# Kernel tuning notes

Hardware: AMD Instinct MI355X
Metric: run time of the kernel (lower is better)

The kernel has to match this reference:

```python
import jax, jax.numpy as jnp
import numpy as np

NEG_INF = -1e9

def _build_tables():
    # LC0-style 73-plane encoding per from-square: planes 0..55 queen moves
    # (8 directions x 7 distances), 56..63 knight moves. to_sq[from, plane]
    # is the to-square index; valid marks on-board targets.
    to_sq = np.zeros((64, 64), np.int32)
    valid = np.zeros((64, 64), bool)
    dirs = [(1, 0), (1, 1), (0, 1), (-1, 1), (-1, 0), (-1, -1), (0, -1), (1, -1)]
    knights = [(2, 1), (1, 2), (-1, 2), (-2, 1), (-2, -1), (-1, -2), (1, -2), (2, -1)]
    for sq in range(64):
        r, c = divmod(sq, 8)
        for d, (dr, dc) in enumerate(dirs):
            for dist in range(1, 8):
                p = d * 7 + (dist - 1)
                nr, nc = r + dr * dist, c + dc * dist
                if 0 <= nr < 8 and 0 <= nc < 8:
                    to_sq[sq, p] = nr * 8 + nc
                    valid[sq, p] = True
        for i, (dr, dc) in enumerate(knights):
            nr, nc = r + dr, c + dc
            if 0 <= nr < 8 and 0 <= nc < 8:
                to_sq[sq, 56 + i] = nr * 8 + nc
                valid[sq, 56 + i] = True
    promo_from = (np.arange(64) // 8) == 6  # rank 7 pawns (0-indexed rank 6)
    return to_sq, valid, promo_from

TO_SQ_NP, VALID_NP, PROMO_FROM_NP = _build_tables()
TO_SQ = jnp.asarray(TO_SQ_NP)            # (64, 64) int32
TO_VALID = jnp.asarray(VALID_NP)         # (64, 64) bool
PROMO_FROM = jnp.asarray(PROMO_FROM_NP)  # (64,) bool

EMBED_DIM = 1024
POLICY_DIM = 128
SCALE = POLICY_DIM ** (-0.5)


def setup_inputs() -> dict:
    key = jax.random.key(0)
    ks = jax.random.split(key, 4)
    B = 1024
    std = 1.0 / np.sqrt(EMBED_DIM)
    x = jax.random.normal(ks[0], (B, 64, EMBED_DIM), dtype=jnp.float32)
    Wq = jax.random.normal(ks[1], (EMBED_DIM, POLICY_DIM), dtype=jnp.float32) * std
    Wk = jax.random.normal(ks[2], (EMBED_DIM, POLICY_DIM), dtype=jnp.float32) * std
    Wu = jax.random.normal(ks[3], (EMBED_DIM, 9), dtype=jnp.float32) * std
    bq = jnp.zeros((POLICY_DIM,), jnp.float32)
    bk = jnp.zeros((POLICY_DIM,), jnp.float32)
    bu = jnp.zeros((9,), jnp.float32)
    return {"x": x, "Wq": Wq, "bq": bq, "Wk": Wk, "bk": bk, "Wu": Wu, "bu": bu}


def reference(x, Wq, bq, Wk, bk, Wu, bu):
    b = x.shape[0]
    q = jnp.einsum('bsd,dp->bsp', x, Wq) + bq            # (B, 64, P)
    k = jnp.einsum('bsd,dp->bsp', x, Wk) + bk            # (B, 64, P)
    logits_ft = jnp.einsum('bfp,btp->bft', q, k) * SCALE  # (B, 64, 64)
    # gather to-square logits into plane order per from-square
    idx = jnp.broadcast_to(TO_SQ[None].astype(jnp.int32), (b, 64, 64))
    logits_64 = jnp.take_along_axis(logits_ft, idx, axis=-1)  # (B, 64, 64)
    logits_64 = jnp.where(TO_VALID[None], logits_64, jnp.float32(NEG_INF))
    up = jnp.einsum('bsd,dn->bsn', x, Wu) + bu            # (B, 64, 9)
    up = jnp.where(PROMO_FROM[None, :, None], up, jnp.float32(NEG_INF))
    logits = jnp.concatenate([logits_64, up], axis=-1)    # (B, 64, 73)
    return logits.reshape(b, 64 * 73)
```

## Files before the change

kernel.cpp:

```cpp
#include <hip/hip_runtime.h>

#define NEG_INF (-1e9f)
#define SCALE_F 0.08838834764831845f

typedef __attribute__((ext_vector_type(8))) short short8;
typedef __attribute__((ext_vector_type(4))) float float4v;

__device__ __constant__ int cDR[8] = {1,1,0,-1,-1,-1,0,1};
__device__ __constant__ int cDC[8] = {0,1,1,1,0,-1,-1,-1};
__device__ __constant__ int cKR[8] = {2,1,-1,-2,-2,-1,1,2};
__device__ __constant__ int cKC[8] = {1,2,2,1,-1,-2,-2,-1};

__device__ __forceinline__ ushort f2bf(float f) {
  union { float f; unsigned u; } a; a.f = f;
  unsigned u = a.u;
  return (ushort)((u + 0x7FFFu + ((u >> 16) & 1u)) >> 16);
}

__device__ __forceinline__ short8 pack8(float4 a, float4 b) {
  union { short8 v; unsigned u[4]; } o;
  unsigned a0 = __float_as_uint(a.x), a1 = __float_as_uint(a.y);
  unsigned a2 = __float_as_uint(a.z), a3 = __float_as_uint(a.w);
  unsigned b0 = __float_as_uint(b.x), b1 = __float_as_uint(b.y);
  unsigned b2 = __float_as_uint(b.z), b3 = __float_as_uint(b.w);
  o.u[0] = (a1 & 0xFFFF0000u) | (a0 >> 16);
  o.u[1] = (a3 & 0xFFFF0000u) | (a2 >> 16);
  o.u[2] = (b1 & 0xFFFF0000u) | (b0 >> 16);
  o.u[3] = (b3 & 0xFFFF0000u) | (b2 >> 16);
  return o.v;
}

__global__ void wconv_kernel(const float* __restrict__ Wq,
                             const float* __restrict__ Wk,
                             const float* __restrict__ Wu,
                             ushort* __restrict__ Wsw) {
  int row = blockIdx.x;
  for (int k = threadIdx.x; k < 1024; k += 256) {
    float v;
    if (row < 128)      v = Wq[k * 128 + row];
    else if (row < 256) v = Wk[k * 128 + (row - 128)];
    else if (row < 265) v = Wu[k * 9 + (row - 256)];
    else                v = 0.f;
    int kc = k >> 6, kin = k & 63;
    Wsw[(size_t)kc * 18432 + row * 64 + kin] = f2bf(v);
  }
}

__global__ __launch_bounds__(256, 3)
void apol_main(const float* __restrict__ x,
               const float* __restrict__ bq,
               const float* __restrict__ bk,
               const float* __restrict__ bu,
               const ushort* __restrict__ Wsw,
               float* __restrict__ out) {
  __shared__ __align__(16) char smem[33792];
  char*   xs0 = smem;
  char*   xs1 = smem + 8192;
  ushort* qs  = (ushort*)smem;
  ushort* ks  = (ushort*)(smem + 16896);
  float*  Sl  = (float*)smem;

  const int tid = threadIdx.x;
  const int w = tid >> 6, lane = tid & 63;
  const int l15 = lane & 15, qd = lane >> 4;
  const char* xb = (const char*)(x + (size_t)blockIdx.x * 65536);
  const char* WsB = (const char*)Wsw;

  const int srow = w * 16 + (lane >> 2);
  const int scol4 = lane & 3;
  const char* xsrc = xb + srow * 4096 + scol4 * 64;
  const int wr0 = srow * 128 + (((scol4 * 2 + 0) ^ (srow & 7)) * 16);
  const int wr1 = srow * 128 + (((scol4 * 2 + 1) ^ (srow & 7)) * 16);

  const int arow = l15 * 128;
  int aoff[2];
  #pragma unroll
  for (int kk = 0; kk < 2; ++kk)
    aoff[kk] = (((kk * 4 + qd) ^ (l15 & 7)) * 16);

  const int wvo = (w * 64 + l15) * 128 + qd * 16;
  const int uvo = (256 + l15) * 128 + qd * 16;

  float4v acc[4][4];
  #pragma unroll
  for (int i = 0; i < 4; ++i)
    #pragma unroll
    for (int j = 0; j < 4; ++j)
      acc[i][j] = (float4v){0.f, 0.f, 0.f, 0.f};
  float4v aup = (float4v){0.f, 0.f, 0.f, 0.f};

  {
    float4 g0 = *(const float4*)(xsrc);
    float4 g1 = *(const float4*)(xsrc + 16);
    float4 g2 = *(const float4*)(xsrc + 32);
    float4 g3 = *(const float4*)(xsrc + 48);
    *(short8*)(xs0 + wr0) = pack8(g0, g1);
    *(short8*)(xs0 + wr1) = pack8(g2, g3);
  }
  __syncthreads();

  #pragma unroll 1
  for (int kc = 0; kc < 16; ++kc) {
    const char* xcur = (kc & 1) ? xs1 : xs0;
    char* xnxt = (kc & 1) ? xs0 : xs1;
    float4 g0, g1, g2, g3;
    const bool pf = (kc < 15);
    if (pf) {
      const char* s = xsrc + (kc + 1) * 256;
      g0 = *(const float4*)(s);
      g1 = *(const float4*)(s + 16);
      g2 = *(const float4*)(s + 32);
      g3 = *(const float4*)(s + 48);
    }
    const char* wp = WsB + (size_t)kc * 36864;
    #pragma unroll
    for (int kk = 0; kk < 2; ++kk) {
      short8 bf[4];
      #pragma unroll
      for (int nt = 0; nt < 4; ++nt)
        bf[nt] = *(const short8*)(wp + wvo + nt * 2048 + kk * 64);
      short8 ub;
      if (w == 3) ub = *(const short8*)(wp + uvo + kk * 64);
      #pragma unroll
      for (int mt = 0; mt < 4; ++mt) {
        short8 af = *(const short8*)(xcur + mt * 2048 + arow + aoff[kk]);
        #pragma unroll
        for (int nt = 0; nt < 4; ++nt)
          acc[mt][nt] = __builtin_amdgcn_mfma_f32_16x16x32_bf16(
              af, bf[nt], acc[mt][nt], 0, 0, 0);
        if (w == 3 && mt == 3)
          aup = __builtin_amdgcn_mfma_f32_16x16x32_bf16(af, ub, aup, 0, 0, 0);
      }
    }
    if (pf) {
      *(short8*)(xnxt + wr0) = pack8(g0, g1);
      *(short8*)(xnxt + wr1) = pack8(g2, g3);
    }
    __syncthreads();
  }

  float* outb = out + (size_t)blockIdx.x * 4672;

  if (w == 3 && qd < 2 && l15 < 9) {
    float bias = bu[l15];
    #pragma unroll
    for (int r = 0; r < 4; ++r) {
      int f = 48 + qd * 4 + r;
      outb[f * 73 + 64 + l15] = aup[r] + bias;
    }
  }

  #pragma unroll
  for (int nt = 0; nt < 4; ++nt) {
    int C = w * 64 + nt * 16 + l15;
    bool isq = (C < 128);
    int p = isq ? C : (C - 128);
    float bias = isq ? bq[p] : bk[p];
    ushort* dstb = isq ? qs : ks;
    #pragma unroll
    for (int mt = 0; mt < 4; ++mt)
      #pragma unroll
      for (int r = 0; r < 4; ++r) {
        int row = mt * 16 + qd * 4 + r;
        float v = acc[mt][nt][r] + bias;
        if (isq) v *= SCALE_F;
        dstb[row * 132 + p] = f2bf(v);
      }
  }
  __syncthreads();

  float4v acc2[4];
  #pragma unroll
  for (int nt = 0; nt < 4; ++nt) acc2[nt] = (float4v){0.f, 0.f, 0.f, 0.f};
  #pragma unroll
  for (int kp = 0; kp < 4; ++kp) {
    int kb = kp * 32 + qd * 8;
    short8 a2 = *(const short8*)((const char*)&qs[(w * 16 + l15) * 132 + kb]);
    #pragma unroll
    for (int nt = 0; nt < 4; ++nt) {
      short8 b2 = *(const short8*)((const char*)&ks[(nt * 16 + l15) * 132 + kb]);
      acc2[nt] = __builtin_amdgcn_mfma_f32_16x16x32_bf16(a2, b2, acc2[nt], 0, 0, 0);
    }
  }
  __syncthreads();
  #pragma unroll
  for (int nt = 0; nt < 4; ++nt)
    #pragma unroll
    for (int r = 0; r < 4; ++r)
      Sl[(w * 16 + qd * 4 + r) * 65 + nt * 16 + l15] = acc2[nt][r];
  __syncthreads();

  for (int idx = tid; idx < 4672; idx += 256) {
    int f = idx / 73;
    int j = idx - f * 73;
    float val;
    if (j < 64) {
      int rr = f >> 3, cc = f & 7;
      int nr, nc;
      if (j < 56) {
        int d = j / 7;
        int dist = j - d * 7 + 1;
        nr = rr + cDR[d] * dist;
        nc = cc + cDC[d] * dist;
      } else {
        nr = rr + cKR[j - 56];
        nc = cc + cKC[j - 56];
      }
      val = (nr >= 0 && nr < 8 && nc >= 0 && nc < 8) ? Sl[f * 65 + nr * 8 + nc]
                                                     : NEG_INF;
    } else {
      if (f >= 48 && f < 56) continue;
      val = NEG_INF;
    }
    outb[idx] = val;
  }
}

extern "C" void kernel_launch(void* const* d_in, const int* in_sizes, int n_in,
                              void* d_out, int out_size, void* d_ws, size_t ws_size,
                              hipStream_t stream) {
  const float* x  = (const float*)d_in[0];
  const float* Wq = (const float*)d_in[1];
  const float* bq = (const float*)d_in[2];
  const float* Wk = (const float*)d_in[3];
  const float* bk = (const float*)d_in[4];
  const float* Wu = (const float*)d_in[5];
  const float* bu = (const float*)d_in[6];
  float* out = (float*)d_out;
  ushort* Wsw = (ushort*)d_ws;

  const int B = in_sizes[0] / 65536;

  wconv_kernel<<<288, 256, 0, stream>>>(Wq, Wk, Wu, Wsw);
  apol_main<<<B, 256, 0, stream>>>(x, bq, bk, bu, Wsw, out);
}
```

Baseline: 470.5 us.

## Register-prefetch weight fragments across K chunks and split promo projection into separate kernel

The main GEMM loop is unrolled by two with ping-pong register buffers, so the next chunk's bf16 weight fragments load while the current chunk's MFMAs run, instead of being loaded right before use. The underpromotion projection, previously an extra MFMA on wave 3 with a divergent branch, moves to a small scalar FP32 kernel that re-reads the 8 promotion rows of x per batch. This lowers per-iteration load latency and the wave-3 imbalance in the main kernel. In exchange it adds register pressure under launch bounds of 3 blocks per SM, plus an extra launch and extra x reads.

```diff
diff --git a/kernel.cpp b/kernel.cpp
--- a/kernel.cpp
+++ b/kernel.cpp
@@ -32,25 +32,37 @@
 
 __global__ void wconv_kernel(const float* __restrict__ Wq,
                              const float* __restrict__ Wk,
-                             const float* __restrict__ Wu,
                              ushort* __restrict__ Wsw) {
   int row = blockIdx.x;
   for (int k = threadIdx.x; k < 1024; k += 256) {
-    float v;
-    if (row < 128)      v = Wq[k * 128 + row];
-    else if (row < 256) v = Wk[k * 128 + (row - 128)];
-    else if (row < 265) v = Wu[k * 9 + (row - 256)];
-    else                v = 0.f;
+    float v = (row < 128) ? Wq[k * 128 + row] : Wk[k * 128 + (row - 128)];
     int kc = k >> 6, kin = k & 63;
     Wsw[(size_t)kc * 18432 + row * 64 + kin] = f2bf(v);
   }
+}
+
+__global__ void apol_promo(const float* __restrict__ x,
+                           const float* __restrict__ Wu,
+                           const float* __restrict__ bu,
+                           float* __restrict__ out) {
+  int b = blockIdx.x;
+  int t = threadIdx.x;
+  if (t >= 72) return;
+  int r = t / 9, c = t - r * 9;
+  const float* xr = x + (size_t)b * 65536 + (48 + r) * 1024;
+  float s = 0.f;
+  for (int d = 0; d < 1024; d += 4) {
+    float4 xv = *(const float4*)(xr + d);
+    s += xv.x * Wu[d * 9 + c] + xv.y * Wu[(d + 1) * 9 + c] +
+         xv.z * Wu[(d + 2) * 9 + c] + xv.w * Wu[(d + 3) * 9 + c];
+  }
+  out[(size_t)b * 4672 + (48 + r) * 73 + 64 + c] = s + bu[c];
 }
 
 __global__ __launch_bounds__(256, 3)
 void apol_main(const float* __restrict__ x,
                const float* __restrict__ bq,
                const float* __restrict__ bk,
-               const float* __restrict__ bu,
                const ushort* __restrict__ Wsw,
                float* __restrict__ out) {
   __shared__ __align__(16) char smem[33792];
@@ -73,13 +85,10 @@
   const int wr1 = srow * 128 + (((scol4 * 2 + 1) ^ (srow & 7)) * 16);
 
   const int arow = l15 * 128;
-  int aoff[2];
-  #pragma unroll
-  for (int kk = 0; kk < 2; ++kk)
-    aoff[kk] = (((kk * 4 + qd) ^ (l15 & 7)) * 16);
+  const int aoff0 = (((0 * 4 + qd) ^ (l15 & 7)) * 16);
+  const int aoff1 = (((1 * 4 + qd) ^ (l15 & 7)) * 16);
 
   const int wvo = (w * 64 + l15) * 128 + qd * 16;
-  const int uvo = (256 + l15) * 128 + qd * 16;
 
   float4v acc[4][4];
   #pragma unroll
@@ -87,68 +96,72 @@
     #pragma unroll
     for (int j = 0; j < 4; ++j)
       acc[i][j] = (float4v){0.f, 0.f, 0.f, 0.f};
-  float4v aup = (float4v){0.f, 0.f, 0.f, 0.f};
-
+
+  short8 bwA[2][4], bwB[2][4];
+  float4 gx0, gx1, gx2, gx3;
+
+  #pragma unroll
+  for (int kk = 0; kk < 2; ++kk)
+    #pragma unroll
+    for (int nt = 0; nt < 4; ++nt)
+      bwA[kk][nt] = *(const short8*)(WsB + wvo + nt * 2048 + kk * 64);
   {
-    float4 g0 = *(const float4*)(xsrc);
-    float4 g1 = *(const float4*)(xsrc + 16);
-    float4 g2 = *(const float4*)(xsrc + 32);
-    float4 g3 = *(const float4*)(xsrc + 48);
-    *(short8*)(xs0 + wr0) = pack8(g0, g1);
-    *(short8*)(xs0 + wr1) = pack8(g2, g3);
-  }
-  __syncthreads();
+    gx0 = *(const float4*)(xsrc);
+    gx1 = *(const float4*)(xsrc + 16);
+    gx2 = *(const float4*)(xsrc + 32);
+    gx3 = *(const float4*)(xsrc + 48);
+    *(short8*)(xs0 + wr0) = pack8(gx0, gx1);
+    *(short8*)(xs0 + wr1) = pack8(gx2, gx3);
+  }
+  __syncthreads();
+
+#define CHUNK_BODY(KC, XCUR, XNXT, BWC, BWN)                                   \
+  {                                                                            \
+    const bool pf = (KC) < 15;                                                 \
+    if (pf) {                                                                  \
+      const char* wpn = WsB + (size_t)((KC) + 1) * 36864;                      \
+      _Pragma("unroll")                                                        \
+      for (int kk = 0; kk < 2; ++kk)                                           \
+        _Pragma("unroll")                                                      \
+        for (int nt = 0; nt < 4; ++nt)                                         \
+          BWN[kk][nt] = *(const short8*)(wpn + wvo + nt * 2048 + kk * 64);     \
+      const char* s = xsrc + ((KC) + 1) * 256;                                 \
+      gx0 = *(const float4*)(s);                                               \
+      gx1 = *(const float4*)(s + 16);                                          \
+      gx2 = *(const float4*)(s + 32);                                          \
+      gx3 = *(const float4*)(s + 48);                                          \
+    }                                                                          \
+    _Pragma("unroll")                                                          \
+    for (int mt = 0; mt < 4; ++mt) {                                           \
+      short8 af0 = *(const short8*)((XCUR) + mt * 2048 + arow + aoff0);        \
+      _Pragma("unroll")                                                        \
+      for (int nt = 0; nt < 4; ++nt)                                           \
+        acc[mt][nt] = __builtin_amdgcn_mfma_f32_16x16x32_bf16(                 \
+            af0, BWC[0][nt], acc[mt][nt], 0, 0, 0);                            \
+    }                                                                          \
+    _Pragma("unroll")                                                          \
+    for (int mt = 0; mt < 4; ++mt) {                                           \
+      short8 af1 = *(const short8*)((XCUR) + mt * 2048 + arow + aoff1);        \
+      _Pragma("unroll")                                                        \
+      for (int nt = 0; nt < 4; ++nt)                                           \
+        acc[mt][nt] = __builtin_amdgcn_mfma_f32_16x16x32_bf16(                 \
+            af1, BWC[1][nt], acc[mt][nt], 0, 0, 0);                            \
+    }                                                                          \
+    if (pf) {                                                                  \
+      *(short8*)((XNXT) + wr0) = pack8(gx0, gx1);                              \
+      *(short8*)((XNXT) + wr1) = pack8(gx2, gx3);                              \
+    }                                                                          \
+    __syncthreads();                                                           \
+  }
 
   #pragma unroll 1
-  for (int kc = 0; kc < 16; ++kc) {
-    const char* xcur = (kc & 1) ? xs1 : xs0;
-    char* xnxt = (kc & 1) ? xs0 : xs1;
-    float4 g0, g1, g2, g3;
-    const bool pf = (kc < 15);
-    if (pf) {
-      const char* s = xsrc + (kc + 1) * 256;
-      g0 = *(const float4*)(s);
-      g1 = *(const float4*)(s + 16);
-      g2 = *(const float4*)(s + 32);
-      g3 = *(const float4*)(s + 48);
-    }
-    const char* wp = WsB + (size_t)kc * 36864;
-    #pragma unroll
-    for (int kk = 0; kk < 2; ++kk) {
-      short8 bf[4];
-      #pragma unroll
-      for (int nt = 0; nt < 4; ++nt)
-        bf[nt] = *(const short8*)(wp + wvo + nt * 2048 + kk * 64);
-      short8 ub;
-      if (w == 3) ub = *(const short8*)(wp + uvo + kk * 64);
-      #pragma unroll
-      for (int mt = 0; mt < 4; ++mt) {
-        short8 af = *(const short8*)(xcur + mt * 2048 + arow + aoff[kk]);
-        #pragma unroll
-        for (int nt = 0; nt < 4; ++nt)
-          acc[mt][nt] = __builtin_amdgcn_mfma_f32_16x16x32_bf16(
-              af, bf[nt], acc[mt][nt], 0, 0, 0);
-        if (w == 3 && mt == 3)
-          aup = __builtin_amdgcn_mfma_f32_16x16x32_bf16(af, ub, aup, 0, 0, 0);
-      }
-    }
-    if (pf) {
-      *(short8*)(xnxt + wr0) = pack8(g0, g1);
-      *(short8*)(xnxt + wr1) = pack8(g2, g3);
-    }
-    __syncthreads();
-  }
+  for (int kc = 0; kc < 16; kc += 2) {
+    CHUNK_BODY(kc, xs0, xs1, bwA, bwB)
+    CHUNK_BODY(kc + 1, xs1, xs0, bwB, bwA)
+  }
+#undef CHUNK_BODY
 
   float* outb = out + (size_t)blockIdx.x * 4672;
-
-  if (w == 3 && qd < 2 && l15 < 9) {
-    float bias = bu[l15];
-    #pragma unroll
-    for (int r = 0; r < 4; ++r) {
-      int f = 48 + qd * 4 + r;
-      outb[f * 73 + 64 + l15] = aup[r] + bias;
-    }
-  }
 
   #pragma unroll
   for (int nt = 0; nt < 4; ++nt) {
@@ -231,6 +244,7 @@
 
   const int B = in_sizes[0] / 65536;
 
-  wconv_kernel<<<288, 256, 0, stream>>>(Wq, Wk, Wu, Wsw);
-  apol_main<<<B, 256, 0, stream>>>(x, bq, bk, bu, Wsw, out);
-}
+  wconv_kernel<<<256, 256, 0, stream>>>(Wq, Wk, Wsw);
+  apol_promo<<<B, 128, 0, stream>>>(x, Wu, bu, out);
+  apol_main<<<B, 256, 0, stream>>>(x, bq, bk, Wsw, out);
+}
```

Measured after the change: 503.8 us. 1.07x slower.

## Stage x in two large half-K chunks instead of a 16-step double buffer

Applied to the files above, without the earlier changes.

Replaces the 16-iteration double-buffered x staging (64-element K chunks with a register prefetch) with two phases. Each phase loads half of K (512 columns, 64 KB of bf16) into LDS with wide, coalesced row reads, then runs eight MFMA K-steps without a barrier between them. This cuts barrier count and gives contiguous per-row loads. In exchange, LDS use grows to 64 KB, launch bounds drop to 2 blocks per CU, and loads no longer overlap with compute inside a block.

```diff
diff --git a/kernel.cpp b/kernel.cpp
--- a/kernel.cpp
+++ b/kernel.cpp
@@ -46,16 +46,15 @@
   }
 }
 
-__global__ __launch_bounds__(256, 3)
+__global__ __launch_bounds__(256, 2)
 void apol_main(const float* __restrict__ x,
                const float* __restrict__ bq,
                const float* __restrict__ bk,
                const float* __restrict__ bu,
                const ushort* __restrict__ Wsw,
                float* __restrict__ out) {
-  __shared__ __align__(16) char smem[33792];
-  char*   xs0 = smem;
-  char*   xs1 = smem + 8192;
+  __shared__ __align__(16) char smem[65536];
+  char*   xs  = smem;
   ushort* qs  = (ushort*)smem;
   ushort* ks  = (ushort*)(smem + 16896);
   float*  Sl  = (float*)smem;
@@ -66,17 +65,8 @@
   const char* xb = (const char*)(x + (size_t)blockIdx.x * 65536);
   const char* WsB = (const char*)Wsw;
 
-  const int srow = w * 16 + (lane >> 2);
-  const int scol4 = lane & 3;
-  const char* xsrc = xb + srow * 4096 + scol4 * 64;
-  const int wr0 = srow * 128 + (((scol4 * 2 + 0) ^ (srow & 7)) * 16);
-  const int wr1 = srow * 128 + (((scol4 * 2 + 1) ^ (srow & 7)) * 16);
-
-  const int arow = l15 * 128;
-  int aoff[2];
-  #pragma unroll
-  for (int kk = 0; kk < 2; ++kk)
-    aoff[kk] = (((kk * 4 + qd) ^ (l15 & 7)) * 16);
+  const int arow = l15 * 1024;
+  const int axor = l15 & 7;
 
   const int wvo = (w * 64 + l15) * 128 + qd * 16;
   const int uvo = (256 + l15) * 128 + qd * 16;
@@ -89,55 +79,45 @@
       acc[i][j] = (float4v){0.f, 0.f, 0.f, 0.f};
   float4v aup = (float4v){0.f, 0.f, 0.f, 0.f};
 
-  {
-    float4 g0 = *(const float4*)(xsrc);
-    float4 g1 = *(const float4*)(xsrc + 16);
-    float4 g2 = *(const float4*)(xsrc + 32);
-    float4 g3 = *(const float4*)(xsrc + 48);
-    *(short8*)(xs0 + wr0) = pack8(g0, g1);
-    *(short8*)(xs0 + wr1) = pack8(g2, g3);
-  }
-  __syncthreads();
-
-  #pragma unroll 1
-  for (int kc = 0; kc < 16; ++kc) {
-    const char* xcur = (kc & 1) ? xs1 : xs0;
-    char* xnxt = (kc & 1) ? xs0 : xs1;
-    float4 g0, g1, g2, g3;
-    const bool pf = (kc < 15);
-    if (pf) {
-      const char* s = xsrc + (kc + 1) * 256;
-      g0 = *(const float4*)(s);
-      g1 = *(const float4*)(s + 16);
-      g2 = *(const float4*)(s + 32);
-      g3 = *(const float4*)(s + 48);
-    }
-    const char* wp = WsB + (size_t)kc * 36864;
-    #pragma unroll
-    for (int kk = 0; kk < 2; ++kk) {
-      short8 bf[4];
+  for (int h = 0; h < 2; ++h) {
+    if (h) __syncthreads();
+    #pragma unroll 8
+    for (int j = 0; j < 16; ++j) {
+      int row = j * 4 + w;
+      const char* s = xb + row * 4096 + h * 2048 + lane * 32;
+      float4 g0 = *(const float4*)(s);
+      float4 g1 = *(const float4*)(s + 16);
+      *(short8*)(xs + row * 1024 + ((lane ^ (row & 7)) * 16)) = pack8(g0, g1);
+    }
+    __syncthreads();
+
+    const char* wh = WsB + (size_t)h * 8 * 36864;
+    #pragma unroll 2
+    for (int kc8 = 0; kc8 < 8; ++kc8) {
+      const char* wp = wh + kc8 * 36864;
       #pragma unroll
-      for (int nt = 0; nt < 4; ++nt)
-        bf[nt] = *(const short8*)(wp + wvo + nt * 2048 + kk * 64);
-      short8 ub;
-      if (w == 3) ub = *(const short8*)(wp + uvo + kk * 64);
-      #pragma unroll
-      for (int mt = 0; mt < 4; ++mt) {
-        short8 af = *(const short8*)(xcur + mt * 2048 + arow + aoff[kk]);
+      for (int kk = 0; kk < 2; ++kk) {
+        short8 bf[4];
         #pragma unroll
         for (int nt = 0; nt < 4; ++nt)
-          acc[mt][nt] = __builtin_amdgcn_mfma_f32_16x16x32_bf16(
-              af, bf[nt], acc[mt][nt], 0, 0, 0);
-        if (w == 3 && mt == 3)
-          aup = __builtin_amdgcn_mfma_f32_16x16x32_bf16(af, ub, aup, 0, 0, 0);
+          bf[nt] = *(const short8*)(wp + wvo + nt * 2048 + kk * 64);
+        short8 ub;
+        if (w == 3) ub = *(const short8*)(wp + uvo + kk * 64);
+        #pragma unroll
+        for (int mt = 0; mt < 4; ++mt) {
+          short8 af = *(const short8*)(
+              xs + mt * 16384 + arow + (((kc8 * 8 + kk * 4 + qd) ^ axor) * 16));
+          #pragma unroll
+          for (int nt = 0; nt < 4; ++nt)
+            acc[mt][nt] = __builtin_amdgcn_mfma_f32_16x16x32_bf16(
+                af, bf[nt], acc[mt][nt], 0, 0, 0);
+          if (w == 3 && mt == 3)
+            aup = __builtin_amdgcn_mfma_f32_16x16x32_bf16(af, ub, aup, 0, 0, 0);
+        }
       }
     }
-    if (pf) {
-      *(short8*)(xnxt + wr0) = pack8(g0, g1);
-      *(short8*)(xnxt + wr1) = pack8(g2, g3);
-    }
-    __syncthreads();
-  }
+  }
+  __syncthreads();
 
   float* outb = out + (size_t)blockIdx.x * 4672;
 
```

Measured after the change: 447.8 us. -4.8%, faster.
